# Kernel optimization log

Hardware: AMD Instinct MI355X
Metric: run time of the kernel (lower is better)

Reference implementation:

```python
import jax, jax.numpy as jnp
import numpy as np

B, H, W, D = 8, 128, 128, 64


def setup_inputs() -> dict:
    key = jax.random.key(0)
    k1, k2, k3, k4, k5, k6 = jax.random.split(key, 6)
    x = jax.random.normal(k1, (B, H, W, D), dtype=jnp.float32)
    atten_x_full = jax.random.normal(k2, (B, H, W, W), dtype=jnp.float32)
    atten_y_full = jax.random.normal(k3, (B, W, H, H), dtype=jnp.float32)
    value_full = jax.random.normal(k4, (B, H, W, D), dtype=jnp.float32)
    # nn.Parameter init: bias = -|randn|, shift = |randn|
    shift = jnp.abs(jax.random.normal(k5, (1,), dtype=jnp.float32))
    bias = -jnp.abs(jax.random.normal(k6, (1,), dtype=jnp.float32))
    return {"x": x, "atten_x_full": atten_x_full, "atten_y_full": atten_y_full,
            "value_full": value_full, "shift": shift, "bias": bias}


def reference(x, atten_x_full, atten_y_full, value_full, shift, bias):
    Hh, Ww = x.shape[1], x.shape[2]
    # squared axial distances: dx2[c, j] = (j - c)^2, dy2[r, i] = (i - r)^2
    jw = jnp.arange(Ww, dtype=jnp.float32)
    ih = jnp.arange(Hh, dtype=jnp.float32)
    dx2 = (jw[None, :] - jw[:, None]) ** 2  # [W, W]
    dy2 = (ih[None, :] - ih[:, None]) ** 2  # [H, H]
    # dis = -(shift * d^2 + bias); logits = dis + atten
    logits_x = atten_x_full - (shift[0] * dx2 + bias[0])  # [B,H,W,W] (dx2 broadcasts over c=axis2, j=axis3)
    logits_y = atten_y_full - (shift[0] * dy2 + bias[0])  # [B,W,H,H] (dy2 over r=axis2, i=axis3)
    ax = jax.nn.softmax(logits_x, axis=-1)  # attention along row r (over columns j)
    ay = jax.nn.softmax(logits_y, axis=-1)  # attention along column c (over rows i)
    # out[b,r,c,d] = sum_j ax[b,r,c,j] * v[b,r,j,d] + sum_i ay[b,c,r,i] * v[b,i,c,d]
    out = (jnp.einsum('brcj,brjd->brcd', ax, value_full)
           + jnp.einsum('bcri,bicd->brcd', ay, value_full))
    return out
```

## Files before the change

### kernel.cpp

```cpp
#include <hip/hip_runtime.h>
#include <stdint.h>

typedef _Float16 half4_t __attribute__((ext_vector_type(4)));
typedef float    floatx4 __attribute__((ext_vector_type(4)));

static constexpr int HW = 128;
static constexpr int DD = 64;

#define GLOAD4O(dst, ptr, o) asm volatile("global_load_dwordx4 %0, %1, off offset:" #o : "=v"(dst) : "v"(ptr) : "memory")
#define GLOAD1O(dst, ptr, o) asm volatile("global_load_dword %0, %1, off offset:" #o   : "=v"(dst) : "v"(ptr) : "memory")
#define WAITV(n) do { asm volatile("s_waitcnt vmcnt(" #n ")" ::: "memory"); \
                      __builtin_amdgcn_sched_barrier(0); } while (0)

#define LOADT(t_, dst) do { \
    const float* p0_ = vX + (size_t)(16*(t_) + 4*g + 0) * vstr; \
    const float* p1_ = vX + (size_t)(16*(t_) + 4*g + 1) * vstr; \
    const float* p2_ = vX + (size_t)(16*(t_) + 4*g + 2) * vstr; \
    const float* p3_ = vX + (size_t)(16*(t_) + 4*g + 3) * vstr; \
    GLOAD1O(dst[0][0], p0_, 0); GLOAD1O(dst[0][1], p0_, 64); GLOAD1O(dst[0][2], p0_, 128); GLOAD1O(dst[0][3], p0_, 192); \
    GLOAD1O(dst[1][0], p1_, 0); GLOAD1O(dst[1][1], p1_, 64); GLOAD1O(dst[1][2], p1_, 128); GLOAD1O(dst[1][3], p1_, 192); \
    GLOAD1O(dst[2][0], p2_, 0); GLOAD1O(dst[2][1], p2_, 64); GLOAD1O(dst[2][2], p2_, 128); GLOAD1O(dst[2][3], p2_, 192); \
    GLOAD1O(dst[3][0], p3_, 0); GLOAD1O(dst[3][1], p3_, 64); GLOAD1O(dst[3][2], p3_, 128); GLOAD1O(dst[3][3], p3_, 192); \
} while (0)

#define CVT1(vf_, c_) do { _Pragma("unroll") for (int dt = 0; dt < 4; ++dt) { \
        vf_[dt][0] = (_Float16)c_[0][dt]; \
        vf_[dt][1] = (_Float16)c_[1][dt]; \
        vf_[dt][2] = (_Float16)c_[2][dt]; \
        vf_[dt][3] = (_Float16)c_[3][dt]; } } while (0)

#define MFMA1(vf_, t_) do { _Pragma("unroll") for (int dt = 0; dt < 4; ++dt) \
        acc[dt] = __builtin_amdgcn_mfma_f32_16x16x16f16(vf_[dt], af[(t_)], acc[dt], 0, 0, 0); } while (0)

template<bool IS_Y>
__global__ __launch_bounds__(256, 3)
void axial_attn(const float* __restrict__ atten,
                const float* __restrict__ vsrc,
                const float* __restrict__ shift_p,
                float* __restrict__ out)
{
    const int blk  = blockIdx.x;
    const int h    = blk & 1;
    const int brc  = blk >> 1;
    const int b    = brc >> 7;
    const int rc   = brc & 127;
    const int tid  = threadIdx.x;
    const int w    = tid >> 6;
    const int lane = tid & 63;
    const int lr   = lane & 15;
    const int g    = lane >> 4;
    const int grow = h * 64 + w * 16 + lr;

    const float* arow = atten + (size_t)brc * (HW * HW) + (size_t)grow * HW + g * 4;
    floatx4 a0, a1, a2, a3, a4, a5, a6, a7;
    GLOAD4O(a0, arow, 0);   GLOAD4O(a1, arow, 64);  GLOAD4O(a2, arow, 128); GLOAD4O(a3, arow, 192);
    GLOAD4O(a4, arow, 256); GLOAD4O(a5, arow, 320); GLOAD4O(a6, arow, 384); GLOAD4O(a7, arow, 448);

    const float* vX   = IS_Y ? vsrc + ((size_t)b * HW * HW + rc) * DD + lr
                             : vsrc + (size_t)brc * (HW * DD) + lr;
    const int    vstr = IS_Y ? HW * DD : DD;

    float* ob = IS_Y ? out + (size_t)b * (HW * HW * DD) + (size_t)grow * (HW * DD) + rc * DD
                     : out + (size_t)brc * (HW * DD) + (size_t)grow * DD;
    floatx4 acc[4];
    if (IS_Y) {
        const float* pb = ob + 4 * g;
        GLOAD4O(acc[0], pb, 0); GLOAD4O(acc[1], pb, 64);
        GLOAD4O(acc[2], pb, 128); GLOAD4O(acc[3], pb, 192);
    } else {
        #pragma unroll
        for (int dt = 0; dt < 4; ++dt) acc[dt] = (floatx4)(0.f);
    }

    float cb0[4][4], cb1[4][4], cb2[4][4], cb3[4][4];
    LOADT(0, cb0); LOADT(1, cb1);

    if constexpr (IS_Y) { WAITV(36); } else { WAITV(32); }

    LOADT(2, cb2); LOADT(3, cb3);

    const float shift = shift_p[0];

    floatx4 av[8] = {a0, a1, a2, a3, a4, a5, a6, a7};
    #pragma unroll
    for (int t = 0; t < 8; ++t)
        #pragma unroll
        for (int i = 0; i < 4; ++i) {
            const float d = (float)(16 * t + 4 * g + i - grow);
            av[t][i] = fmaf(-shift * d, d, av[t][i]);
        }
    float m16[16];
    #pragma unroll
    for (int i = 0; i < 16; ++i) m16[i] = fmaxf(av[i >> 2][i & 3], av[4 + (i >> 2)][i & 3]);
    #pragma unroll
    for (int s = 8; s >= 1; s >>= 1)
        #pragma unroll
        for (int i = 0; i < s; ++i) m16[i] = fmaxf(m16[i], m16[i + s]);
    float mx = m16[0];
    mx = fmaxf(mx, __shfl_xor(mx, 16));
    mx = fmaxf(mx, __shfl_xor(mx, 32));

    float e[32];
    #pragma unroll
    for (int t = 0; t < 8; ++t)
        #pragma unroll
        for (int i = 0; i < 4; ++i) e[t * 4 + i] = __expf(av[t][i] - mx);
    float s16[16];
    #pragma unroll
    for (int i = 0; i < 16; ++i) s16[i] = e[i] + e[i + 16];
    #pragma unroll
    for (int s = 8; s >= 1; s >>= 1)
        #pragma unroll
        for (int i = 0; i < s; ++i) s16[i] += s16[i + s];
    float sum = s16[0];
    sum += __shfl_xor(sum, 16);
    sum += __shfl_xor(sum, 32);
    const float inv = 1.0f / sum;

    half4_t af[8];
    #pragma unroll
    for (int t = 0; t < 8; ++t)
        #pragma unroll
        for (int i = 0; i < 4; ++i)
            af[t][i] = (_Float16)(e[4 * t + i] * inv);

    half4_t vf[4];
    WAITV(48); CVT1(vf, cb0); MFMA1(vf, 0); LOADT(4, cb0);
    WAITV(48); CVT1(vf, cb1); MFMA1(vf, 1); LOADT(5, cb1);
    WAITV(48); CVT1(vf, cb2); MFMA1(vf, 2); LOADT(6, cb2);
    WAITV(48); CVT1(vf, cb3); MFMA1(vf, 3); LOADT(7, cb3);
    WAITV(48); CVT1(vf, cb0); MFMA1(vf, 4);
    WAITV(32); CVT1(vf, cb1); MFMA1(vf, 5);
    WAITV(16); CVT1(vf, cb2); MFMA1(vf, 6);
    WAITV(0);  CVT1(vf, cb3); MFMA1(vf, 7);

    #pragma unroll
    for (int dt = 0; dt < 4; ++dt)
        *(floatx4*)&ob[16 * dt + 4 * g] = acc[dt];
}

extern "C" void kernel_launch(void* const* d_in, const int* in_sizes, int n_in,
                              void* d_out, int out_size, void* d_ws, size_t ws_size,
                              hipStream_t stream)
{
    const float* atx   = (const float*)d_in[1];
    const float* aty   = (const float*)d_in[2];
    const float* val   = (const float*)d_in[3];
    const float* shift = (const float*)d_in[4];
    float* out = (float*)d_out;

    axial_attn<false><<<dim3(8 * 128 * 2), dim3(256), 0, stream>>>(atx, val, shift, out);
    axial_attn<true ><<<dim3(8 * 128 * 2), dim3(256), 0, stream>>>(aty, val, shift, out);
}
```

Baseline: 60.02 us.

## Prefetch Y-attention into cache during X pass and reorder block indexing

The X-pass kernel now loads its block's slice of the Y attention tensor (32 KB per block) after finishing its own work and discards the values. This is meant to warm the large last-level cache so the following Y-pass kernel reads atten_y from cache rather than HBM. Block index decoding is also reordered so that batch varies fastest, which changes how work is spread across CUs and the order of memory accesses. The cost is extra load traffic and latency in the X pass, and the prefetch only helps if the data stays cached between the two launches.

```diff
diff --git a/kernel.cpp b/kernel.cpp
--- a/kernel.cpp
+++ b/kernel.cpp
@@ -37,13 +37,14 @@
 void axial_attn(const float* __restrict__ atten,
                 const float* __restrict__ vsrc,
                 const float* __restrict__ shift_p,
-                float* __restrict__ out)
+                float* __restrict__ out,
+                const float* __restrict__ pf)
 {
-    const int blk  = blockIdx.x;
-    const int h    = blk & 1;
-    const int brc  = blk >> 1;
-    const int b    = brc >> 7;
-    const int rc   = brc & 127;
+    const int bid  = blockIdx.x;
+    const int b    = bid & 7;
+    const int h    = (bid >> 3) & 1;
+    const int rc   = bid >> 4;
+    const int brc  = (b << 7) | rc;
     const int tid  = threadIdx.x;
     const int w    = tid >> 6;
     const int lane = tid & 63;
@@ -137,6 +138,21 @@
     #pragma unroll
     for (int dt = 0; dt < 4; ++dt)
         *(floatx4*)&ob[16 * dt + 4 * g] = acc[dt];
+
+    if constexpr (!IS_Y) {
+        const float* ps = pf + (size_t)bid * 8192 + tid * 4;
+        floatx4 p0, p1, p2, p3, p4, p5, p6, p7;
+        GLOAD4O(p0, ps, 0);
+        GLOAD4O(p1, (ps + 1024), 0);
+        GLOAD4O(p2, (ps + 2048), 0);
+        GLOAD4O(p3, (ps + 3072), 0);
+        GLOAD4O(p4, (ps + 4096), 0);
+        GLOAD4O(p5, (ps + 5120), 0);
+        GLOAD4O(p6, (ps + 6144), 0);
+        GLOAD4O(p7, (ps + 7168), 0);
+        asm volatile("" :: "v"(p0), "v"(p1), "v"(p2), "v"(p3),
+                           "v"(p4), "v"(p5), "v"(p6), "v"(p7));
+    }
 }
 
 extern "C" void kernel_launch(void* const* d_in, const int* in_sizes, int n_in,
@@ -149,6 +165,6 @@
     const float* shift = (const float*)d_in[4];
     float* out = (float*)d_out;
 
-    axial_attn<false><<<dim3(8 * 128 * 2), dim3(256), 0, stream>>>(atx, val, shift, out);
-    axial_attn<true ><<<dim3(8 * 128 * 2), dim3(256), 0, stream>>>(aty, val, shift, out);
+    axial_attn<false><<<dim3(8 * 128 * 2), dim3(256), 0, stream>>>(atx, val, shift, out, aty);
+    axial_attn<true ><<<dim3(8 * 128 * 2), dim3(256), 0, stream>>>(aty, val, shift, out, aty);
 }
```

Result: slower. 62.06 us (+3.4%).

## Fuse X and Y axial kernels into one launch using atomic accumulation

Applied to the files above, without the earlier changes.

Merges the two separate axial-attention launches into one grid where alternate blocks handle the X or Y direction. Both contributions are accumulated into the output with per-element float atomicAdd after a memset zeroes the buffer. The Y pass no longer reads back the partial output. The prefetch schedule is also reshaped to keep fewer value tiles in flight. The cost is an extra memset pass, 16 scalar atomics per thread instead of vector stores, and nondeterministic float summation order.

```diff
diff --git a/kernel.cpp b/kernel.cpp
--- a/kernel.cpp
+++ b/kernel.cpp
@@ -32,16 +32,18 @@
 #define MFMA1(vf_, t_) do { _Pragma("unroll") for (int dt = 0; dt < 4; ++dt) \
         acc[dt] = __builtin_amdgcn_mfma_f32_16x16x16f16(vf_[dt], af[(t_)], acc[dt], 0, 0, 0); } while (0)
 
-template<bool IS_Y>
 __global__ __launch_bounds__(256, 3)
-void axial_attn(const float* __restrict__ atten,
-                const float* __restrict__ vsrc,
-                const float* __restrict__ shift_p,
-                float* __restrict__ out)
+void axial_fused(const float* __restrict__ atx,
+                 const float* __restrict__ aty,
+                 const float* __restrict__ vsrc,
+                 const float* __restrict__ shift_p,
+                 float* __restrict__ out)
 {
-    const int blk  = blockIdx.x;
-    const int h    = blk & 1;
-    const int brc  = blk >> 1;
+    const int bid  = blockIdx.x;
+    const int isy  = bid & 1;
+    const int rest = bid >> 1;
+    const int h    = rest & 1;
+    const int brc  = rest >> 1;
     const int b    = brc >> 7;
     const int rc   = brc & 127;
     const int tid  = threadIdx.x;
@@ -51,33 +53,22 @@
     const int g    = lane >> 4;
     const int grow = h * 64 + w * 16 + lr;
 
-    const float* arow = atten + (size_t)brc * (HW * HW) + (size_t)grow * HW + g * 4;
+    const float* atten = isy ? aty : atx;
+    const float* arow  = atten + (size_t)brc * (HW * HW) + (size_t)grow * HW + g * 4;
     floatx4 a0, a1, a2, a3, a4, a5, a6, a7;
     GLOAD4O(a0, arow, 0);   GLOAD4O(a1, arow, 64);  GLOAD4O(a2, arow, 128); GLOAD4O(a3, arow, 192);
     GLOAD4O(a4, arow, 256); GLOAD4O(a5, arow, 320); GLOAD4O(a6, arow, 384); GLOAD4O(a7, arow, 448);
 
-    const float* vX   = IS_Y ? vsrc + ((size_t)b * HW * HW + rc) * DD + lr
-                             : vsrc + (size_t)brc * (HW * DD) + lr;
-    const int    vstr = IS_Y ? HW * DD : DD;
-
-    float* ob = IS_Y ? out + (size_t)b * (HW * HW * DD) + (size_t)grow * (HW * DD) + rc * DD
-                     : out + (size_t)brc * (HW * DD) + (size_t)grow * DD;
-    floatx4 acc[4];
-    if (IS_Y) {
-        const float* pb = ob + 4 * g;
-        GLOAD4O(acc[0], pb, 0); GLOAD4O(acc[1], pb, 64);
-        GLOAD4O(acc[2], pb, 128); GLOAD4O(acc[3], pb, 192);
-    } else {
-        #pragma unroll
-        for (int dt = 0; dt < 4; ++dt) acc[dt] = (floatx4)(0.f);
-    }
+    const float* vX   = isy ? vsrc + ((size_t)b * HW * HW + rc) * DD + lr
+                            : vsrc + (size_t)brc * (HW * DD) + lr;
+    const int    vstr = isy ? HW * DD : DD;
+    float* ob = isy ? out + (size_t)b * (HW * HW * DD) + (size_t)grow * (HW * DD) + rc * DD
+                    : out + (size_t)brc * (HW * DD) + (size_t)grow * DD;
 
     float cb0[4][4], cb1[4][4], cb2[4][4], cb3[4][4];
     LOADT(0, cb0); LOADT(1, cb1);
 
-    if constexpr (IS_Y) { WAITV(36); } else { WAITV(32); }
-
-    LOADT(2, cb2); LOADT(3, cb3);
+    WAITV(32);
 
     const float shift = shift_p[0];
 
@@ -117,6 +108,8 @@
     sum += __shfl_xor(sum, 32);
     const float inv = 1.0f / sum;
 
+    LOADT(2, cb2);
+
     half4_t af[8];
     #pragma unroll
     for (int t = 0; t < 8; ++t)
@@ -124,19 +117,25 @@
         for (int i = 0; i < 4; ++i)
             af[t][i] = (_Float16)(e[4 * t + i] * inv);
 
+    floatx4 acc[4];
+    #pragma unroll
+    for (int dt = 0; dt < 4; ++dt) acc[dt] = (floatx4)(0.f);
+
     half4_t vf[4];
-    WAITV(48); CVT1(vf, cb0); MFMA1(vf, 0); LOADT(4, cb0);
-    WAITV(48); CVT1(vf, cb1); MFMA1(vf, 1); LOADT(5, cb1);
-    WAITV(48); CVT1(vf, cb2); MFMA1(vf, 2); LOADT(6, cb2);
-    WAITV(48); CVT1(vf, cb3); MFMA1(vf, 3); LOADT(7, cb3);
-    WAITV(48); CVT1(vf, cb0); MFMA1(vf, 4);
+    WAITV(32); CVT1(vf, cb0); MFMA1(vf, 0); LOADT(3, cb3);
+    WAITV(32); CVT1(vf, cb1); MFMA1(vf, 1); LOADT(4, cb0);
+    WAITV(32); CVT1(vf, cb2); MFMA1(vf, 2); LOADT(5, cb1);
+    WAITV(32); CVT1(vf, cb3); MFMA1(vf, 3); LOADT(6, cb2);
+    WAITV(32); CVT1(vf, cb0); MFMA1(vf, 4); LOADT(7, cb3);
     WAITV(32); CVT1(vf, cb1); MFMA1(vf, 5);
     WAITV(16); CVT1(vf, cb2); MFMA1(vf, 6);
     WAITV(0);  CVT1(vf, cb3); MFMA1(vf, 7);
 
     #pragma unroll
     for (int dt = 0; dt < 4; ++dt)
-        *(floatx4*)&ob[16 * dt + 4 * g] = acc[dt];
+        #pragma unroll
+        for (int i = 0; i < 4; ++i)
+            atomicAdd(&ob[16 * dt + 4 * g + i], acc[dt][i]);
 }
 
 extern "C" void kernel_launch(void* const* d_in, const int* in_sizes, int n_in,
@@ -149,6 +148,6 @@
     const float* shift = (const float*)d_in[4];
     float* out = (float*)d_out;
 
-    axial_attn<false><<<dim3(8 * 128 * 2), dim3(256), 0, stream>>>(atx, val, shift, out);
-    axial_attn<true ><<<dim3(8 * 128 * 2), dim3(256), 0, stream>>>(aty, val, shift, out);
+    hipMemsetAsync(out, 0, (size_t)out_size * sizeof(float), stream);
+    axial_fused<<<dim3(8 * 128 * 2 * 2), dim3(256), 0, stream>>>(atx, aty, val, shift, out);
 }
```

Result: slower. 228.8 us (+281.2%).
